# Kernel tuning notes

Measured on AMD Instinct MI355X. Metric: run time of the kernel, lower is better.

Reference implementation:

```python
import jax, jax.numpy as jnp
import numpy as np

D_MODEL = 1024
NUM_HEADS = 16
D_HEAD = D_MODEL // NUM_HEADS
MAX_SEQ_LEN = 2048
THETA = 10000.0
BATCH = 2
SEQ = 2048


def _rope_tables():
    # inv_freq over even dims; emb interleaves each freq twice: [f0,f0,f1,f1,...]
    inv_freq = 1.0 / (THETA ** (jnp.arange(0, D_HEAD, 2, dtype=jnp.float32) / D_HEAD))
    t = jnp.arange(MAX_SEQ_LEN, dtype=jnp.float32)
    freqs = jnp.einsum('i,j->ij', t, inv_freq)  # [S, d_head/2]
    emb = jnp.stack((freqs, freqs), axis=-1).reshape(MAX_SEQ_LEN, D_HEAD)
    return jnp.cos(emb), jnp.sin(emb)


def _rotate_half(x):
    # pairwise interleaved rotation: (x0,x1,x2,x3,...) -> (-x1,x0,-x3,x2,...)
    xr = x.reshape(x.shape[:-1] + (D_HEAD // 2, 2))
    x1, x2 = xr[..., 0], xr[..., 1]
    return jnp.stack((-x2, x1), axis=-1).reshape(x.shape)


def setup_inputs() -> dict:
    key = jax.random.key(0)
    ks = jax.random.split(key, 5)
    std = np.sqrt(2.0 / (D_MODEL + D_MODEL)).astype(np.float32)
    return {
        'in_features': jax.random.normal(ks[0], (BATCH, SEQ, D_MODEL), dtype=jnp.float32),
        'token_positions': jnp.arange(SEQ, dtype=jnp.int64) if jax.config.jax_enable_x64 else jnp.arange(SEQ, dtype=jnp.int32),
        'wq': jax.random.normal(ks[1], (D_MODEL, D_MODEL), dtype=jnp.float32) * std,
        'wk': jax.random.normal(ks[2], (D_MODEL, D_MODEL), dtype=jnp.float32) * std,
        'wv': jax.random.normal(ks[3], (D_MODEL, D_MODEL), dtype=jnp.float32) * std,
        'wo': jax.random.normal(ks[4], (D_MODEL, D_MODEL), dtype=jnp.float32) * std,
    }


def reference(in_features, token_positions, wq, wk, wv, wo):
    b, s, _ = in_features.shape
    cos_tab, sin_tab = _rope_tables()
    cos = cos_tab[token_positions]  # [s, d_head]
    sin = sin_tab[token_positions]

    def split_heads(t):  # [b, s, d_model] -> [b, h, s, d_head]
        return t.reshape(b, s, NUM_HEADS, D_HEAD).transpose(0, 2, 1, 3)

    q = split_heads(jnp.einsum('bsd,ed->bse', in_features, wq))
    k = split_heads(jnp.einsum('bsd,ed->bse', in_features, wk))
    v = split_heads(jnp.einsum('bsd,ed->bse', in_features, wv))

    q = q * cos + _rotate_half(q) * sin
    k = k * cos + _rotate_half(k) * sin

    scale = 1.0 / np.sqrt(D_HEAD).astype(np.float32)
    scores = jnp.einsum('bhqd,bhkd->bhqk', q, k) * scale  # [b,h,s,s]
    causal = jnp.tril(jnp.ones((s, s), dtype=bool))
    scores = jnp.where(causal, scores, -jnp.inf)
    weights = jax.nn.softmax(scores, axis=-1)
    out = jnp.einsum('bhqk,bhkd->bhqd', weights, v)
    out = out.transpose(0, 2, 1, 3).reshape(b, s, D_MODEL)
    return jnp.einsum('bsd,ed->bse', out, wo)
```

## Files before the change

kernel.cpp:

```cpp
#include <hip/hip_runtime.h>


typedef __attribute__((ext_vector_type(8))) short bf16x8;
typedef __attribute__((ext_vector_type(4))) float f32x4;

__device__ __forceinline__ short f2bf(float f) {
  unsigned u = __float_as_uint(f);
  unsigned r = (u + 0x7fffu + ((u >> 16) & 1u)) >> 16;
  return (short)(r & 0xFFFFu);
}

__device__ __forceinline__ unsigned pk2(float a, float b) {
  return __builtin_amdgcn_perm(__float_as_uint(b) + 0x8000u,
                               __float_as_uint(a) + 0x8000u, 0x07060302u);
}

__device__ __forceinline__ void async16(const void* g, void* l) {
  __builtin_amdgcn_global_load_lds(
      (const __attribute__((address_space(1))) void*)g,
      (__attribute__((address_space(3))) void*)l, 16, 0, 0);
}

__device__ __forceinline__ void cstore(short* C, size_t i, float v) { C[i] = f2bf(v); }
__device__ __forceinline__ void cstore(float* C, size_t i, float v) { C[i] = v; }

__global__ void cast_all(const float4* __restrict__ X,
                         const float4* __restrict__ w0, const float4* __restrict__ w1,
                         const float4* __restrict__ w2, const float4* __restrict__ w3,
                         short* __restrict__ Xb, short* __restrict__ Wb) {
  int t = blockIdx.x * 256 + threadIdx.x;
  const float4* s;
  short4* d;
  if (t < (1 << 20)) {
    s = X + t; d = (short4*)Xb + t;
  } else {
    int u = t - (1 << 20);
    int which = u >> 18;
    s = ((which == 0) ? w0 : (which == 1) ? w1 : (which == 2) ? w2 : w3) + (u & 0x3FFFF);
    d = (short4*)Wb + u;
  }
  float4 v = *s;
  *d = make_short4(f2bf(v.x), f2bf(v.y), f2bf(v.z), f2bf(v.w));
}

enum EpiMode { EPI_ROW, EPI_KFRAG, EPI_VFRAG };

template <typename OUT, int MR, int NR, bool ROPE, EpiMode EM>
__device__ __forceinline__ void gemm_core(short* __restrict__ As, short* __restrict__ Bs,
                                          const short* __restrict__ A, const short* __restrict__ B,
                                          OUT* __restrict__ C, int bm, int bn, int ldc,
                                          const int* __restrict__ pos) {
  constexpr int BM = 32 * MR, BN = 32 * NR;
  const int tid  = threadIdx.x;
  const int lane = tid & 63, wave = tid >> 6;
  const int col  = lane & 15, quad = lane >> 4;
  const int wm = (wave & 1) * (16 * MR), wn = (wave >> 1) * (16 * NR);

  f32x4 acc[MR][NR];
#pragma unroll
  for (int i = 0; i < MR; i++)
#pragma unroll
    for (int j = 0; j < NR; j++) acc[i][j] = (f32x4){0.f, 0.f, 0.f, 0.f};

  auto stage = [&](int k0, int bu) {
#pragma unroll
    for (int c = tid; c < BM * 4; c += 256) {
      int r = c >> 2, cc = (c & 3) << 3;
      async16(A + (size_t)(bm + r) * 1024 + k0 + cc, As + bu * BM * 32 + c * 8);
    }
#pragma unroll
    for (int c = tid; c < BN * 4; c += 256) {
      int r = c >> 2, cc = (c & 3) << 3;
      async16(B + (size_t)(bn + r) * 1024 + k0 + cc, Bs + bu * BN * 32 + c * 8);
    }
  };

  stage(0, 0);
  for (int it = 0; it < 32; ++it) {
    __syncthreads();
    if (it < 31) stage((it + 1) * 32, (it + 1) & 1);
    const short* as = As + (it & 1) * BM * 32;
    const short* bs = Bs + (it & 1) * BN * 32;

    bf16x8 af[MR], bfr[NR];
#pragma unroll
    for (int i = 0; i < MR; i++)
      af[i] = *(const bf16x8*)(as + (wm + i * 16 + col) * 32 + quad * 8);
#pragma unroll
    for (int i = 0; i < NR; i++)
      bfr[i] = *(const bf16x8*)(bs + (wn + i * 16 + col) * 32 + quad * 8);
#pragma unroll
    for (int mi = 0; mi < MR; mi++)
#pragma unroll
      for (int ni = 0; ni < NR; ni++)
        acc[mi][ni] = __builtin_amdgcn_mfma_f32_16x16x32_bf16(af[mi], bfr[ni], acc[mi][ni], 0, 0, 0);
  }

  if (ROPE) {
    float invf_rev[NR];
#pragma unroll
    for (int ni = 0; ni < NR; ni++) {
      int pr = ((bn + wn + ni * 16 + col) & 63) >> 1;
      invf_rev[ni] = exp2f(-0.4152410118609203f * (float)pr) * 0.15915494309189535f;
    }
    const float sgn = (col & 1) ? 1.f : -1.f;
#pragma unroll
    for (int mi = 0; mi < MR; mi++) {
#pragma unroll
      for (int r = 0; r < 4; r++) {
        int row = bm + wm + mi * 16 + quad * 4 + r;
        float fp = (float)pos[row & 2047];
#pragma unroll
        for (int ni = 0; ni < NR; ni++) {
          float rev = fp * invf_rev[ni];
          rev -= floorf(rev);
          float sn = __builtin_amdgcn_sinf(rev);
          float cs = __builtin_amdgcn_cosf(rev);
          float x  = acc[mi][ni][r];
          float px = __shfl_xor(x, 1);
          acc[mi][ni][r] = fmaf(x, cs, sgn * px * sn);
        }
      }
    }
  }

  if (EM == EPI_ROW) {
#pragma unroll
    for (int mi = 0; mi < MR; mi++) {
#pragma unroll
      for (int r = 0; r < 4; r++) {
        size_t row = (size_t)(bm + wm + mi * 16 + quad * 4 + r);
#pragma unroll
        for (int ni = 0; ni < NR; ni++) {
          int cg = bn + wn + ni * 16 + col;
          cstore(C, row * ldc + cg, acc[mi][ni][r]);
        }
      }
    }
  } else if (EM == EPI_KFRAG) {
#pragma unroll
    for (int mi = 0; mi < MR; mi++) {
#pragma unroll
      for (int r = 0; r < 4; r++) {
        int m = bm + wm + mi * 16 + quad * 4 + r;
        int bq = m >> 11, key = m & 2047;
        int kt = key >> 6, nb = (key >> 4) & 3, cl = key & 15;
#pragma unroll
        for (int ni = 0; ni < NR; ni++) {
          int e = bn + wn + ni * 16 + col;
          int h = e >> 6, d = e & 63;
          size_t seg = ((((size_t)(bq * 16 + h) * 32 + kt) * 4 + nb) * 2 + (d >> 5));
          cstore((short*)C, seg * 512 + (((d >> 3) & 3) * 16 + cl) * 8 + (d & 7), acc[mi][ni][r]);
        }
      }
    }
  } else {
#pragma unroll
    for (int mi = 0; mi < MR; mi++) {
#pragma unroll
      for (int r = 0; r < 4; r++) {
        int e = bm + wm + mi * 16 + quad * 4 + r;
        int h = e >> 6, d = e & 63;
        int nb = d >> 4, cl = d & 15;
#pragma unroll
        for (int ni = 0; ni < NR; ni++) {
          int m = bn + wn + ni * 16 + col;
          int bq = m >> 11, key = m & 2047;
          int kt = key >> 6, k64 = key & 63;
          size_t seg = ((((size_t)(bq * 16 + h) * 32 + kt) * 4 + nb) * 2 + (k64 >> 5));
          cstore((short*)C, seg * 512 + (((k64 >> 3) & 3) * 16 + cl) * 8 + (k64 & 7), acc[mi][ni][r]);
        }
      }
    }
  }
}

__global__ __launch_bounds__(256) void qkv_gemm(const short* __restrict__ Xb,
                                                const short* __restrict__ Wq,
                                                const short* __restrict__ Wk,
                                                const short* __restrict__ Wv,
                                                short* __restrict__ Qo,
                                                short* __restrict__ Kf,
                                                short* __restrict__ Vf,
                                                const int* __restrict__ pos) {
  __shared__ __align__(16) short sm[2 * 128 * 32 + 2 * 128 * 32];
  short* As = sm;
  short* Bs = sm + 2 * 128 * 32;
  const int z = blockIdx.z;
  if (z == 0)      gemm_core<short, 4, 4, true,  EPI_ROW  >(As, Bs, Xb, Wq, Qo, blockIdx.x * 128, blockIdx.y * 128, 1024, pos);
  else if (z == 1) gemm_core<short, 4, 4, true,  EPI_KFRAG>(As, Bs, Xb, Wk, Kf, blockIdx.x * 128, blockIdx.y * 128, 0, pos);
  else             gemm_core<short, 4, 4, false, EPI_VFRAG>(As, Bs, Wv, Xb, Vf, blockIdx.y * 128, blockIdx.x * 128, 0, pos);
}

__global__ __launch_bounds__(256) void out_gemm(const short* __restrict__ Ctx,
                                                const short* __restrict__ Wo,
                                                float* __restrict__ C) {
  __shared__ __align__(16) short sm[2 * 64 * 32 + 2 * 128 * 32];
  gemm_core<float, 2, 4, false, EPI_ROW>(sm, sm + 2 * 64 * 32, Ctx, Wo, C,
                                         blockIdx.x * 64, blockIdx.y * 128, 1024, nullptr);
}

__global__ __launch_bounds__(256, 2) void flash_attn(const short* __restrict__ Q,
                                                     const short* __restrict__ Kf,
                                                     const short* __restrict__ Vf,
                                                     short* __restrict__ ctx) {
  const int p = blockIdx.y;
  const int bh = blockIdx.x;
  const int b = bh >> 4, h = bh & 15;
  __shared__ __align__(16) short Ps[4][16 * 72];
  const int tid = threadIdx.x, lane = tid & 63, wave = tid >> 6;
  const int col = lane & 15, quad = lane >> 4;

  const short* Kfb = Kf + (size_t)bh * 131072 + lane * 8;
  const short* Vfb = Vf + (size_t)bh * 131072 + lane * 8;

  const float C1 = 0.18033688011112042f;
  const float C2 = 17.31234049066756f;

  short* myPs = &Ps[wave][0];
  const int cx = col & 3;
  const int pswr0 = col * 72 + ((0 ^ cx) << 4) + quad * 4;
  const int pswr1 = col * 72 + ((1 ^ cx) << 4) + quad * 4;
  const int pswr2 = col * 72 + ((2 ^ cx) << 4) + quad * 4;
  const int pswr3 = col * 72 + ((3 ^ cx) << 4) + quad * 4;
  const int psrd0 = col * 72 + (((quad >> 1) ^ cx) << 4) + (quad & 1) * 8;
  const int psrd1 = col * 72 + ((((quad >> 1) + 2) ^ cx) << 4) + (quad & 1) * 8;

  auto ldk = [&](int kt, bf16x8 (&kf)[4][2]) {
    const int base = kt * 4096;
#pragma unroll
    for (int nb = 0; nb < 4; nb++) {
      kf[nb][0] = *(const bf16x8*)(Kfb + base + (nb * 2 + 0) * 512);
      kf[nb][1] = *(const bf16x8*)(Kfb + base + (nb * 2 + 1) * 512);
    }
  };
  auto ldv = [&](int kt, bf16x8 (&vf)[4][2]) {
    const int base = kt * 4096;
#pragma unroll
    for (int nb = 0; nb < 4; nb++) {
      vf[nb][0] = *(const bf16x8*)(Vfb + base + (nb * 2 + 0) * 512);
      vf[nb][1] = *(const bf16x8*)(Vfb + base + (nb * 2 + 1) * 512);
    }
  };

  auto process = [&](int qt) {
    const size_t qrow = (size_t)(b * 2048 + qt * 64 + wave * 16 + col);
    bf16x8 qf0 = *(const bf16x8*)(Q + qrow * 1024 + h * 64 + quad * 8);
    bf16x8 qf1 = *(const bf16x8*)(Q + qrow * 1024 + h * 64 + 32 + quad * 8);

    float l_i = 0.f;
    f32x4 o_acc[4];
#pragma unroll
    for (int i = 0; i < 4; i++) o_acc[i] = (f32x4){0.f, 0.f, 0.f, 0.f};

    const int qg = qt * 64 + wave * 16 + col;
    bf16x8 kf[4][2], vf[4][2];
    ldk(0, kf);

    for (int kt = 0; kt <= qt; ++kt) {
      ldv(kt, vf);
      f32x4 s_acc[4];
#pragma unroll
      for (int nb = 0; nb < 4; nb++) {
        f32x4 z = (f32x4){0.f, 0.f, 0.f, 0.f};
        z = __builtin_amdgcn_mfma_f32_16x16x32_bf16(kf[nb][0], qf0, z, 0, 0, 0);
        z = __builtin_amdgcn_mfma_f32_16x16x32_bf16(kf[nb][1], qf1, z, 0, 0, 0);
        s_acc[nb] = z;
      }
      if (kt < qt) ldk(kt + 1, kf);
      const bool diag = (kt == qt);
#pragma unroll
      for (int nb = 0; nb < 4; nb++) {
        float pv[4];
#pragma unroll
        for (int r = 0; r < 4; r++) {
          pv[r] = exp2f(s_acc[nb][r] * C1 - C2);
          if (diag && (kt * 64 + nb * 16 + quad * 4 + r) > qg) pv[r] = 0.f;
          l_i += pv[r];
        }
        int wr = (nb == 0) ? pswr0 : (nb == 1) ? pswr1 : (nb == 2) ? pswr2 : pswr3;
        *(uint2*)(myPs + wr) = make_uint2(pk2(pv[0], pv[1]), pk2(pv[2], pv[3]));
      }
      bf16x8 af0 = *(const bf16x8*)(myPs + psrd0);
      bf16x8 af1 = *(const bf16x8*)(myPs + psrd1);
#pragma unroll
      for (int nb = 0; nb < 4; nb++) {
        o_acc[nb] = __builtin_amdgcn_mfma_f32_16x16x32_bf16(af0, vf[nb][0], o_acc[nb], 0, 0, 0);
        o_acc[nb] = __builtin_amdgcn_mfma_f32_16x16x32_bf16(af1, vf[nb][1], o_acc[nb], 0, 0, 0);
      }
    }

    l_i += __shfl_xor(l_i, 16);
    l_i += __shfl_xor(l_i, 32);
    float invl = 1.0f / l_i;

#pragma unroll
    for (int r = 0; r < 4; r++) {
      float inv = __shfl(invl, quad * 4 + r);
      size_t row = (size_t)(b * 2048 + qt * 64 + wave * 16 + quad * 4 + r);
#pragma unroll
      for (int nb = 0; nb < 4; nb++)
        ctx[row * 1024 + h * 64 + nb * 16 + col] = f2bf(o_acc[nb][r] * inv);
    }
  };

  process(p);
  process(31 - p);
}

extern "C" void kernel_launch(void* const* d_in, const int* in_sizes, int n_in,
                              void* d_out, int out_size, void* d_ws, size_t ws_size,
                              hipStream_t stream) {
  const float* X  = (const float*)d_in[0];
  const int* pos  = (const int*)d_in[1];
  const float* wq = (const float*)d_in[2];
  const float* wk = (const float*)d_in[3];
  const float* wv = (const float*)d_in[4];
  const float* wo = (const float*)d_in[5];
  float* out = (float*)d_out;

  short* Xb  = (short*)d_ws;
  short* Wqb = Xb + (1 << 22);
  short* Wkb = Wqb + (1 << 20);
  short* Wvb = Wkb + (1 << 20);
  short* Wob = Wvb + (1 << 20);
  short* Qb  = Wob + (1 << 20);
  short* Kfb = Qb + (1 << 22);
  short* Vfb = Kfb + (1 << 22);
  short* Ctx = Vfb + (1 << 22);

  cast_all<<<8192, 256, 0, stream>>>((const float4*)X, (const float4*)wq, (const float4*)wk,
                                     (const float4*)wv, (const float4*)wo, Xb, Wqb);
  qkv_gemm<<<dim3(32, 8, 3), 256, 0, stream>>>(Xb, Wqb, Wkb, Wvb, Qb, Kfb, Vfb, pos);
  flash_attn<<<dim3(32, 16), 256, 0, stream>>>(Qb, Kfb, Vfb, Ctx);
  out_gemm<<<dim3(64, 8), 256, 0, stream>>>(Ctx, Wob, out);
}
```

Measured before the change: 182.8 us.

## Interleave paired query tiles in flash attention sharing K/V loads, shrink GEMM tiles

Flash attention now processes its two query tiles (p and 31-p) together in one key loop, so each K/V fragment load feeds both tiles instead of being reloaded per tile. Q is written in the same fragment layout as K, giving coalesced fragment loads. Block-to-tile mapping is reordered, and the QKV and output GEMMs use 64-wide N tiles with twice as many blocks to raise occupancy. The cost is higher register pressure from two accumulator sets and more GEMM blocks re-reading A tiles.

```diff
diff --git a/kernel.cpp b/kernel.cpp
--- a/kernel.cpp
+++ b/kernel.cpp
@@ -179,45 +179,63 @@
                                                 const short* __restrict__ Wq,
                                                 const short* __restrict__ Wk,
                                                 const short* __restrict__ Wv,
-                                                short* __restrict__ Qo,
+                                                short* __restrict__ Qf,
                                                 short* __restrict__ Kf,
                                                 short* __restrict__ Vf,
                                                 const int* __restrict__ pos) {
-  __shared__ __align__(16) short sm[2 * 128 * 32 + 2 * 128 * 32];
+  __shared__ __align__(16) short sm[2 * 128 * 32 + 2 * 64 * 32];
   short* As = sm;
   short* Bs = sm + 2 * 128 * 32;
   const int z = blockIdx.z;
-  if (z == 0)      gemm_core<short, 4, 4, true,  EPI_ROW  >(As, Bs, Xb, Wq, Qo, blockIdx.x * 128, blockIdx.y * 128, 1024, pos);
-  else if (z == 1) gemm_core<short, 4, 4, true,  EPI_KFRAG>(As, Bs, Xb, Wk, Kf, blockIdx.x * 128, blockIdx.y * 128, 0, pos);
-  else             gemm_core<short, 4, 4, false, EPI_VFRAG>(As, Bs, Wv, Xb, Vf, blockIdx.y * 128, blockIdx.x * 128, 0, pos);
+  const int x = blockIdx.x, y = blockIdx.y;
+  if (z == 0)      gemm_core<short, 4, 2, true,  EPI_KFRAG>(As, Bs, Xb, Wq, Qf, x * 128, y * 64, 0, pos);
+  else if (z == 1) gemm_core<short, 4, 2, true,  EPI_KFRAG>(As, Bs, Xb, Wk, Kf, x * 128, y * 64, 0, pos);
+  else             gemm_core<short, 4, 2, false, EPI_VFRAG>(As, Bs, Wv, Xb, Vf,
+                                                            (y >> 1) * 128, (x * 2 + (y & 1)) * 64, 0, pos);
 }
 
 __global__ __launch_bounds__(256) void out_gemm(const short* __restrict__ Ctx,
                                                 const short* __restrict__ Wo,
                                                 float* __restrict__ C) {
-  __shared__ __align__(16) short sm[2 * 64 * 32 + 2 * 128 * 32];
-  gemm_core<float, 2, 4, false, EPI_ROW>(sm, sm + 2 * 64 * 32, Ctx, Wo, C,
-                                         blockIdx.x * 64, blockIdx.y * 128, 1024, nullptr);
-}
-
-__global__ __launch_bounds__(256, 2) void flash_attn(const short* __restrict__ Q,
+  __shared__ __align__(16) short sm[2 * 64 * 32 + 2 * 64 * 32];
+  gemm_core<float, 2, 2, false, EPI_ROW>(sm, sm + 2 * 64 * 32, Ctx, Wo, C,
+                                         blockIdx.x * 64, blockIdx.y * 64, 1024, nullptr);
+}
+
+__global__ __launch_bounds__(256, 2) void flash_attn(const short* __restrict__ Qf,
                                                      const short* __restrict__ Kf,
                                                      const short* __restrict__ Vf,
                                                      short* __restrict__ ctx) {
-  const int p = blockIdx.y;
+  const int y = blockIdx.y;
+  const int p = (y < 8) ? y : 23 - y;
+  const int qtA = p, qtB = 31 - p;
   const int bh = blockIdx.x;
   const int b = bh >> 4, h = bh & 15;
-  __shared__ __align__(16) short Ps[4][16 * 72];
+  __shared__ __align__(16) short Ps[8][16 * 72];
   const int tid = threadIdx.x, lane = tid & 63, wave = tid >> 6;
   const int col = lane & 15, quad = lane >> 4;
 
   const short* Kfb = Kf + (size_t)bh * 131072 + lane * 8;
   const short* Vfb = Vf + (size_t)bh * 131072 + lane * 8;
+  const short* Qfb = Qf + (size_t)bh * 131072 + lane * 8 + wave * 1024;
+
+  bf16x8 qA0 = *(const bf16x8*)(Qfb + qtA * 4096);
+  bf16x8 qA1 = *(const bf16x8*)(Qfb + qtA * 4096 + 512);
+  bf16x8 qB0 = *(const bf16x8*)(Qfb + qtB * 4096);
+  bf16x8 qB1 = *(const bf16x8*)(Qfb + qtB * 4096 + 512);
+
+  float lA = 0.f, lB = 0.f;
+  f32x4 oA[4], oB[4];
+#pragma unroll
+  for (int i = 0; i < 4; i++) { oA[i] = (f32x4){0.f, 0.f, 0.f, 0.f}; oB[i] = (f32x4){0.f, 0.f, 0.f, 0.f}; }
 
   const float C1 = 0.18033688011112042f;
   const float C2 = 17.31234049066756f;
-
-  short* myPs = &Ps[wave][0];
+  const int qgA = qtA * 64 + wave * 16 + col;
+  const int qgB = qtB * 64 + wave * 16 + col;
+
+  short* PsA = &Ps[wave * 2 + 0][0];
+  short* PsB = &Ps[wave * 2 + 1][0];
   const int cx = col & 3;
   const int pswr0 = col * 72 + ((0 ^ cx) << 4) + quad * 4;
   const int pswr1 = col * 72 + ((1 ^ cx) << 4) + quad * 4;
@@ -243,69 +261,94 @@
     }
   };
 
-  auto process = [&](int qt) {
-    const size_t qrow = (size_t)(b * 2048 + qt * 64 + wave * 16 + col);
-    bf16x8 qf0 = *(const bf16x8*)(Q + qrow * 1024 + h * 64 + quad * 8);
-    bf16x8 qf1 = *(const bf16x8*)(Q + qrow * 1024 + h * 64 + 32 + quad * 8);
-
-    float l_i = 0.f;
-    f32x4 o_acc[4];
-#pragma unroll
-    for (int i = 0; i < 4; i++) o_acc[i] = (f32x4){0.f, 0.f, 0.f, 0.f};
-
-    const int qg = qt * 64 + wave * 16 + col;
-    bf16x8 kf[4][2], vf[4][2];
-    ldk(0, kf);
-
-    for (int kt = 0; kt <= qt; ++kt) {
-      ldv(kt, vf);
-      f32x4 s_acc[4];
+  bf16x8 kf[4][2], vf[4][2];
+  ldk(0, kf);
+
+  for (int kt = 0; kt <= qtB; ++kt) {
+    ldv(kt, vf);
+    f32x4 sB[4];
+#pragma unroll
+    for (int nb = 0; nb < 4; nb++) {
+      f32x4 z = (f32x4){0.f, 0.f, 0.f, 0.f};
+      z = __builtin_amdgcn_mfma_f32_16x16x32_bf16(kf[nb][0], qB0, z, 0, 0, 0);
+      z = __builtin_amdgcn_mfma_f32_16x16x32_bf16(kf[nb][1], qB1, z, 0, 0, 0);
+      sB[nb] = z;
+    }
+    const bool aAct = (kt <= qtA);
+    f32x4 sA[4];
+    if (aAct) {
 #pragma unroll
       for (int nb = 0; nb < 4; nb++) {
         f32x4 z = (f32x4){0.f, 0.f, 0.f, 0.f};
-        z = __builtin_amdgcn_mfma_f32_16x16x32_bf16(kf[nb][0], qf0, z, 0, 0, 0);
-        z = __builtin_amdgcn_mfma_f32_16x16x32_bf16(kf[nb][1], qf1, z, 0, 0, 0);
-        s_acc[nb] = z;
-      }
-      if (kt < qt) ldk(kt + 1, kf);
-      const bool diag = (kt == qt);
+        z = __builtin_amdgcn_mfma_f32_16x16x32_bf16(kf[nb][0], qA0, z, 0, 0, 0);
+        z = __builtin_amdgcn_mfma_f32_16x16x32_bf16(kf[nb][1], qA1, z, 0, 0, 0);
+        sA[nb] = z;
+      }
+    }
+    if (kt < qtB) ldk(kt + 1, kf);
+
+    {
+      const bool diag = (kt == qtB);
 #pragma unroll
       for (int nb = 0; nb < 4; nb++) {
         float pv[4];
 #pragma unroll
         for (int r = 0; r < 4; r++) {
-          pv[r] = exp2f(s_acc[nb][r] * C1 - C2);
-          if (diag && (kt * 64 + nb * 16 + quad * 4 + r) > qg) pv[r] = 0.f;
-          l_i += pv[r];
+          pv[r] = exp2f(sB[nb][r] * C1 - C2);
+          if (diag && (kt * 64 + nb * 16 + quad * 4 + r) > qgB) pv[r] = 0.f;
+          lB += pv[r];
         }
         int wr = (nb == 0) ? pswr0 : (nb == 1) ? pswr1 : (nb == 2) ? pswr2 : pswr3;
-        *(uint2*)(myPs + wr) = make_uint2(pk2(pv[0], pv[1]), pk2(pv[2], pv[3]));
-      }
-      bf16x8 af0 = *(const bf16x8*)(myPs + psrd0);
-      bf16x8 af1 = *(const bf16x8*)(myPs + psrd1);
-#pragma unroll
-      for (int nb = 0; nb < 4; nb++) {
-        o_acc[nb] = __builtin_amdgcn_mfma_f32_16x16x32_bf16(af0, vf[nb][0], o_acc[nb], 0, 0, 0);
-        o_acc[nb] = __builtin_amdgcn_mfma_f32_16x16x32_bf16(af1, vf[nb][1], o_acc[nb], 0, 0, 0);
-      }
-    }
-
-    l_i += __shfl_xor(l_i, 16);
-    l_i += __shfl_xor(l_i, 32);
-    float invl = 1.0f / l_i;
-
-#pragma unroll
-    for (int r = 0; r < 4; r++) {
-      float inv = __shfl(invl, quad * 4 + r);
-      size_t row = (size_t)(b * 2048 + qt * 64 + wave * 16 + quad * 4 + r);
-#pragma unroll
-      for (int nb = 0; nb < 4; nb++)
-        ctx[row * 1024 + h * 64 + nb * 16 + col] = f2bf(o_acc[nb][r] * inv);
-    }
-  };
-
-  process(p);
-  process(31 - p);
+        *(uint2*)(PsB + wr) = make_uint2(pk2(pv[0], pv[1]), pk2(pv[2], pv[3]));
+      }
+      bf16x8 af0 = *(const bf16x8*)(PsB + psrd0);
+      bf16x8 af1 = *(const bf16x8*)(PsB + psrd1);
+#pragma unroll
+      for (int nb = 0; nb < 4; nb++) {
+        oB[nb] = __builtin_amdgcn_mfma_f32_16x16x32_bf16(af0, vf[nb][0], oB[nb], 0, 0, 0);
+        oB[nb] = __builtin_amdgcn_mfma_f32_16x16x32_bf16(af1, vf[nb][1], oB[nb], 0, 0, 0);
+      }
+    }
+    if (aAct) {
+      const bool diag = (kt == qtA);
+#pragma unroll
+      for (int nb = 0; nb < 4; nb++) {
+        float pv[4];
+#pragma unroll
+        for (int r = 0; r < 4; r++) {
+          pv[r] = exp2f(sA[nb][r] * C1 - C2);
+          if (diag && (kt * 64 + nb * 16 + quad * 4 + r) > qgA) pv[r] = 0.f;
+          lA += pv[r];
+        }
+        int wr = (nb == 0) ? pswr0 : (nb == 1) ? pswr1 : (nb == 2) ? pswr2 : pswr3;
+        *(uint2*)(PsA + wr) = make_uint2(pk2(pv[0], pv[1]), pk2(pv[2], pv[3]));
+      }
+      bf16x8 af0 = *(const bf16x8*)(PsA + psrd0);
+      bf16x8 af1 = *(const bf16x8*)(PsA + psrd1);
+#pragma unroll
+      for (int nb = 0; nb < 4; nb++) {
+        oA[nb] = __builtin_amdgcn_mfma_f32_16x16x32_bf16(af0, vf[nb][0], oA[nb], 0, 0, 0);
+        oA[nb] = __builtin_amdgcn_mfma_f32_16x16x32_bf16(af1, vf[nb][1], oA[nb], 0, 0, 0);
+      }
+    }
+  }
+
+  lA += __shfl_xor(lA, 16);  lA += __shfl_xor(lA, 32);
+  lB += __shfl_xor(lB, 16);  lB += __shfl_xor(lB, 32);
+  float invA = 1.0f / lA, invB = 1.0f / lB;
+
+#pragma unroll
+  for (int r = 0; r < 4; r++) {
+    float ia = __shfl(invA, quad * 4 + r);
+    float ib = __shfl(invB, quad * 4 + r);
+    size_t rowA = (size_t)(b * 2048 + qtA * 64 + wave * 16 + quad * 4 + r);
+    size_t rowB = (size_t)(b * 2048 + qtB * 64 + wave * 16 + quad * 4 + r);
+#pragma unroll
+    for (int nb = 0; nb < 4; nb++) {
+      ctx[rowA * 1024 + h * 64 + nb * 16 + col] = f2bf(oA[nb][r] * ia);
+      ctx[rowB * 1024 + h * 64 + nb * 16 + col] = f2bf(oB[nb][r] * ib);
+    }
+  }
 }
 
 extern "C" void kernel_launch(void* const* d_in, const int* in_sizes, int n_in,
@@ -324,14 +367,14 @@
   short* Wkb = Wqb + (1 << 20);
   short* Wvb = Wkb + (1 << 20);
   short* Wob = Wvb + (1 << 20);
-  short* Qb  = Wob + (1 << 20);
-  short* Kfb = Qb + (1 << 22);
+  short* Qfb = Wob + (1 << 20);
+  short* Kfb = Qfb + (1 << 22);
   short* Vfb = Kfb + (1 << 22);
   short* Ctx = Vfb + (1 << 22);
 
   cast_all<<<8192, 256, 0, stream>>>((const float4*)X, (const float4*)wq, (const float4*)wk,
                                      (const float4*)wv, (const float4*)wo, Xb, Wqb);
-  qkv_gemm<<<dim3(32, 8, 3), 256, 0, stream>>>(Xb, Wqb, Wkb, Wvb, Qb, Kfb, Vfb, pos);
-  flash_attn<<<dim3(32, 16), 256, 0, stream>>>(Qb, Kfb, Vfb, Ctx);
-  out_gemm<<<dim3(64, 8), 256, 0, stream>>>(Ctx, Wob, out);
-}
+  qkv_gemm<<<dim3(32, 16, 3), 256, 0, stream>>>(Xb, Wqb, Wkb, Wvb, Qfb, Kfb, Vfb, pos);
+  flash_attn<<<dim3(32, 16), 256, 0, stream>>>(Qfb, Kfb, Vfb, Ctx);
+  out_gemm<<<dim3(64, 16), 256, 0, stream>>>(Ctx, Wob, out);
+}
```

After: 183.1 us. No clear change (+0.1%).
